# Optimization experiments

Hardware: AMD Instinct MI355X
Metric: run time of the kernel (lower is better)

The kernel has to match this reference:

```python
import jax, jax.numpy as jnp
import numpy as np

B, N, DIM, H, DH = 4, 8192, 1024, 8, 64
INNER = H * DH  # 512


def setup_inputs() -> dict:
    key = jax.random.key(0)
    ks = jax.random.split(key, 6)
    init = lambda k, shape, fan: (jax.random.normal(k, shape, jnp.float32) / np.sqrt(fan).astype(np.float32))
    return {
        "x": jax.random.normal(ks[0], (B, N, DIM), jnp.float32),
        "mask": jnp.ones((B, N), dtype=bool),
        "w_qkv": init(ks[1], (DIM, 3 * INNER), DIM),        # to_qkv (no bias)
        "w_q_logit": init(ks[2], (DH,), DH),                 # to_q_attn_logits
        "w_k_logit": init(ks[3], (DH,), DH),                 # to_k_attn_logits
        "w_r": init(ks[4], (DH, DH), DH),                    # to_r weight
        "b_r": jnp.zeros((DH,), jnp.float32),                # to_r bias
        "w_out": init(ks[5], (INNER, DIM), INNER),           # to_out weight
        "b_out": jnp.zeros((DIM,), jnp.float32),             # to_out bias
    }


def reference(x, mask, w_qkv, w_q_logit, w_k_logit, w_r, b_r, w_out, b_out):
    scale = DH ** -0.5
    neg = -jnp.finfo(x.dtype).max
    qkv = x @ w_qkv                                   # [b, n, 3*inner]
    q, k, v = jnp.split(qkv, 3, axis=-1)
    to_bhnd = lambda t: t.reshape(B, N, H, DH).transpose(0, 2, 1, 3)  # b h n d
    q, k, v = to_bhnd(q), to_bhnd(k), to_bhnd(v)
    m = mask[:, None, :]                              # b 1 n

    # query attention -> global query vector
    q_logits = jnp.einsum('bhnd,d->bhn', q, w_q_logit) * scale
    q_attn = jax.nn.softmax(jnp.where(m, q_logits, neg), axis=-1)
    global_q = jnp.einsum('bhn,bhnd->bhd', q_attn, q)  # b h d

    # key attention conditioned on global query -> global key vector
    k_mod = k * global_q[:, :, None, :]
    k_logits = jnp.einsum('bhnd,d->bhn', k_mod, w_k_logit) * scale
    k_attn = jax.nn.softmax(jnp.where(m, k_logits, neg), axis=-1)
    global_k = jnp.einsum('bhn,bhnd->bhd', k_attn, k)  # (k_aggr = original k)

    # value modulation + residual with q
    u = v * global_k[:, :, None, :]                   # b h n d
    r = jnp.einsum('bhnd,de->bhne', u, w_r) + b_r + q
    r = r.transpose(0, 2, 1, 3).reshape(B, N, INNER)  # b n (h d)
    return r @ w_out + b_out
```

## Files before the change

kernel.cpp:

```cpp
#include <hip/hip_runtime.h>
#include <hip/hip_bf16.h>
#include <cstdint>
#include <cstddef>

#define B_ 4
#define N_ 8192
#define DIM_ 1024
#define H_ 8
#define DH_ 64
#define INNER_ 512
#define QKVW 1536
#define NT_ 32768
#define CH_ 32
#define CROWS 256

typedef __bf16 bf16;
typedef __attribute__((ext_vector_type(8))) __bf16 bf16x8;
typedef __attribute__((ext_vector_type(4))) float f32x4;

__device__ __forceinline__ void gload_lds16(const void* g, void* l) {
  __builtin_amdgcn_global_load_lds((__attribute__((address_space(1))) void*)(g),
                                   (__attribute__((address_space(3))) void*)(l),
                                   16, 0, 0);
}

__global__ void k_convert(const float* __restrict__ src, bf16* __restrict__ dst, int n8) {
  int i = blockIdx.x * blockDim.x + threadIdx.x;
  int stride = gridDim.x * blockDim.x;
  for (; i < n8; i += stride) {
    const float4* p = reinterpret_cast<const float4*>(src) + (size_t)i * 2;
    float4 a = p[0], b = p[1];
    bf16x8 o;
    o[0] = (bf16)a.x; o[1] = (bf16)a.y; o[2] = (bf16)a.z; o[3] = (bf16)a.w;
    o[4] = (bf16)b.x; o[5] = (bf16)b.y; o[6] = (bf16)b.z; o[7] = (bf16)b.w;
    reinterpret_cast<bf16x8*>(dst)[i] = o;
  }
}

__global__ __launch_bounds__(256) void k_transpose_wqkv(const float* __restrict__ w,
                                                        bf16* __restrict__ wt) {
  __shared__ float t[32][33];
  const int n0 = (blockIdx.x % 48) * 32;
  const int k0 = (blockIdx.x / 48) * 32;
  const int c = threadIdx.x & 31, r8 = threadIdx.x >> 5;
#pragma unroll
  for (int i = 0; i < 4; ++i) {
    int rr = r8 + i * 8;
    t[rr][c] = w[(size_t)(k0 + rr) * QKVW + n0 + c];
  }
  __syncthreads();
#pragma unroll
  for (int i = 0; i < 4; ++i) {
    int rr = r8 + i * 8;
    wt[(size_t)(n0 + rr) * DIM_ + k0 + c] = (bf16)t[c][rr];
  }
}

#define BM 128
#define BN 128
#define BK 32

__global__ __launch_bounds__(256, 2) void k_gemm1(const bf16* __restrict__ A,
                                                  const bf16* __restrict__ BT,
                                                  bf16* __restrict__ C) {
  __shared__ bf16 As[BM * BK];
  __shared__ bf16 Bs[BN * BK];
  const int tid = threadIdx.x;
  const int lane = tid & 63;
  const int w = tid >> 6;
  const int wm = w >> 1, wn = w & 1;
  const int flat = blockIdx.y * gridDim.x + blockIdx.x;
  const int idx = (flat & 7) * ((gridDim.x * gridDim.y) >> 3) + (flat >> 3);
  const int m0 = (idx / gridDim.x) * BM;
  const int n0 = (idx % gridDim.x) * BN;
  const int r15 = lane & 15, g = lane >> 4;

  f32x4 acc[4][4] = {};

  for (int kt = 0; kt < DIM_ / BK; ++kt) {
    const int k0 = kt * BK;
#pragma unroll
    for (int i = 0; i < 2; ++i) {
      int f = i * 256 + tid;
      int row = f >> 2, ch = f & 3;
      gload_lds16(A + (size_t)(m0 + row) * DIM_ + k0 + ch * 8,
                  As + (size_t)(i * 256 + w * 64) * 8);
      gload_lds16(BT + (size_t)(n0 + row) * DIM_ + k0 + ch * 8,
                  Bs + (size_t)(i * 256 + w * 64) * 8);
    }
    __syncthreads();
    bf16x8 af[4], bfr[4];
#pragma unroll
    for (int mi = 0; mi < 4; ++mi)
      af[mi] = *reinterpret_cast<const bf16x8*>(As + (wm * 64 + mi * 16 + r15) * BK + g * 8);
#pragma unroll
    for (int ni = 0; ni < 4; ++ni)
      bfr[ni] = *reinterpret_cast<const bf16x8*>(Bs + (wn * 64 + ni * 16 + r15) * BK + g * 8);
#pragma unroll
    for (int mi = 0; mi < 4; ++mi)
#pragma unroll
      for (int ni = 0; ni < 4; ++ni)
        acc[mi][ni] = __builtin_amdgcn_mfma_f32_16x16x32_bf16(af[mi], bfr[ni], acc[mi][ni], 0, 0, 0);
    __syncthreads();
  }

#pragma unroll
  for (int mi = 0; mi < 4; ++mi)
#pragma unroll
    for (int ni = 0; ni < 4; ++ni) {
      int col = n0 + wn * 64 + ni * 16 + r15;
#pragma unroll
      for (int j = 0; j < 4; ++j) {
        int row = m0 + wm * 64 + mi * 16 + g * 4 + j;
        C[(size_t)row * QKVW + col] = (bf16)acc[mi][ni][j];
      }
    }
}

__global__ __launch_bounds__(256) void k_stats_part(const bf16* __restrict__ qkv,
                                                    const float* __restrict__ wql,
                                                    const float* __restrict__ wkl,
                                                    const float* __restrict__ partQ,
                                                    float* __restrict__ part,
                                                    int off, int mode) {
  __shared__ float lgs[CROWS];
  __shared__ float pl[CROWS];
  __shared__ float cfl[DH_];
  __shared__ float redm[4], reds[4];
  __shared__ float vacc[4][DH_];
  const int blk = blockIdx.x;
  const int bh = blk >> 5, ck = blk & 31;
  const int b = bh >> 3, h = bh & 7;
  const bf16* base = qkv + (size_t)(b * N_ + ck * CROWS) * QKVW + h * DH_ + off;
  const int tid = threadIdx.x, lane = tid & 63, w = tid >> 6;

  if (tid < DH_) {
    if (mode == 0) {
      cfl[tid] = wql[tid] * 0.125f;
    } else {
      const float* pp = partQ + (size_t)bh * CH_ * 66;
      float M = -3.4e38f;
#pragma unroll
      for (int c = 0; c < CH_; ++c) M = fmaxf(M, pp[c * 66 + 64]);
      float S = 0.f, v = 0.f;
#pragma unroll
      for (int c = 0; c < CH_; ++c) {
        float e = __expf(pp[c * 66 + 64] - M);
        S += pp[c * 66 + 65] * e;
        v += pp[c * 66 + tid] * e;
      }
      cfl[tid] = wkl[tid] * 0.125f * (v / S);
    }
  }
  __syncthreads();

  const int lr = tid & 7;
  const int rbase = tid >> 3;
  {
    const float c0 = cfl[lr * 8 + 0], c1 = cfl[lr * 8 + 1], c2 = cfl[lr * 8 + 2],
                c3 = cfl[lr * 8 + 3], c4 = cfl[lr * 8 + 4], c5 = cfl[lr * 8 + 5],
                c6 = cfl[lr * 8 + 6], c7 = cfl[lr * 8 + 7];
#pragma unroll
    for (int p = 0; p < 8; ++p) {
      int r = p * 32 + rbase;
      bf16x8 v = *reinterpret_cast<const bf16x8*>(base + (size_t)r * QKVW + lr * 8);
      float s = (float)v[0] * c0 + (float)v[1] * c1 + (float)v[2] * c2 + (float)v[3] * c3 +
                (float)v[4] * c4 + (float)v[5] * c5 + (float)v[6] * c6 + (float)v[7] * c7;
      s += __shfl_xor(s, 1);
      s += __shfl_xor(s, 2);
      s += __shfl_xor(s, 4);
      if (lr == 0) lgs[r] = s;
    }
  }
  __syncthreads();
  const float lg = lgs[tid];
  float m = lg;
#pragma unroll
  for (int d = 1; d < 64; d <<= 1) m = fmaxf(m, __shfl_xor(m, d));
  if (lane == 0) redm[w] = m;
  __syncthreads();
  const float M = fmaxf(fmaxf(redm[0], redm[1]), fmaxf(redm[2], redm[3]));
  float p = __expf(lg - M);
  pl[tid] = p;
  float s = p;
#pragma unroll
  for (int d = 1; d < 64; d <<= 1) s += __shfl_xor(s, d);
  if (lane == 0) reds[w] = s;
  __syncthreads();
  const float S = reds[0] + reds[1] + reds[2] + reds[3];
  float acc = 0.f;
#pragma unroll 8
  for (int r = w; r < CROWS; r += 4)
    acc += pl[r] * (float)base[(size_t)r * QKVW + lane];
  vacc[w][lane] = acc;
  __syncthreads();
  if (tid < DH_) {
    float v = vacc[0][tid] + vacc[1][tid] + vacc[2][tid] + vacc[3][tid];
    float* dst = part + ((size_t)bh * CH_ + ck) * 66;
    dst[tid] = v;
    if (tid == 0) { dst[64] = M; dst[65] = S; }
  }
}

__global__ void k_combine(const float* __restrict__ part, float* __restrict__ outv) {
  const int bh = blockIdx.x, d = threadIdx.x;
  const float* pp = part + (size_t)bh * CH_ * 66;
  float M = -3.4e38f;
#pragma unroll
  for (int c = 0; c < CH_; ++c) M = fmaxf(M, pp[c * 66 + 64]);
  float S = 0.f, v = 0.f;
#pragma unroll
  for (int c = 0; c < CH_; ++c) {
    float e = __expf(pp[c * 66 + 64] - M);
    S += pp[c * 66 + 65] * e;
    v += pp[c * 66 + d] * e;
  }
  outv[bh * DH_ + d] = v / S;
}

__global__ void k_P(const float* __restrict__ wr, const float* __restrict__ wout,
                    float* __restrict__ P) {
  int he = blockIdx.x;
  int h = he >> 6, e = he & 63;
  __shared__ float wrow[DH_];
  if (threadIdx.x < DH_) wrow[threadIdx.x] = wr[e * DH_ + threadIdx.x];
  __syncthreads();
  for (int o = threadIdx.x; o < DIM_; o += 256) {
    float s = 0.f;
#pragma unroll
    for (int d = 0; d < DH_; ++d) s += wrow[d] * wout[(size_t)(h * DH_ + d) * DIM_ + o];
    P[(size_t)he * DIM_ + o] = s;
  }
}

__global__ void k_bo2(const float* __restrict__ br, const float* __restrict__ wout,
                      const float* __restrict__ bout, float* __restrict__ bo2) {
  const int w = threadIdx.x >> 6, lane = threadIdx.x & 63;
  const int o = blockIdx.x * 4 + w;
  float s = 0.f;
#pragma unroll
  for (int j = lane; j < INNER_; j += 64) s += br[lane] * wout[(size_t)j * DIM_ + o];
#pragma unroll
  for (int d = 1; d < 64; d <<= 1) s += __shfl_xor(s, d);
  if (lane == 0) bo2[o] = s + bout[o];
}

__global__ void k_bt(const float* __restrict__ P, const float* __restrict__ gk,
                     const float* __restrict__ wout, bf16* __restrict__ BT) {
  int bo = blockIdx.x;
  int b = bo >> 10, o = bo & 1023;
  bf16* dst = BT + (size_t)bo * DIM_;
  for (int k = threadIdx.x; k < DIM_; k += 256) {
    float v;
    if (k < INNER_) {
      int h = k >> 6, e = k & 63;
      v = gk[(b * H_ + h) * DH_ + e] * P[(size_t)k * DIM_ + o];
    } else {
      v = wout[(size_t)(k - INNER_) * DIM_ + o];
    }
    dst[k] = (bf16)v;
  }
}

__global__ __launch_bounds__(256, 2) void k_gemm2(const bf16* __restrict__ qkv,
                                                  const bf16* __restrict__ BT,
                                                  const float* __restrict__ bo2,
                                                  float* __restrict__ out) {
  __shared__ bf16 As[BM * BK];
  __shared__ bf16 Bs[BN * BK];
  const int tid = threadIdx.x;
  const int lane = tid & 63;
  const int w = tid >> 6;
  const int wm = w >> 1, wn = w & 1;
  const int b = blockIdx.z;
  const int flat = blockIdx.y * gridDim.x + blockIdx.x;
  const int idx = (flat & 7) * ((gridDim.x * gridDim.y) >> 3) + (flat >> 3);
  const int m0 = (idx >> 3) * BM;
  const int n0 = (idx & 7) * BN;
  const int r15 = lane & 15, g = lane >> 4;
  const bf16* BTb = BT + (size_t)b * DIM_ * DIM_;

  f32x4 acc[4][4] = {};

  for (int kt = 0; kt < DIM_ / BK; ++kt) {
    const int k0 = kt * BK;
    const int koff = (k0 < INNER_) ? (2 * INNER_ + k0) : (k0 - INNER_);
#pragma unroll
    for (int i = 0; i < 2; ++i) {
      int f = i * 256 + tid;
      int row = f >> 2, ch = f & 3;
      gload_lds16(qkv + (size_t)(b * N_ + m0 + row) * QKVW + koff + ch * 8,
                  As + (size_t)(i * 256 + w * 64) * 8);
      gload_lds16(BTb + (size_t)(n0 + row) * DIM_ + k0 + ch * 8,
                  Bs + (size_t)(i * 256 + w * 64) * 8);
    }
    __syncthreads();
    bf16x8 af[4], bfr[4];
#pragma unroll
    for (int mi = 0; mi < 4; ++mi)
      af[mi] = *reinterpret_cast<const bf16x8*>(As + (wm * 64 + mi * 16 + r15) * BK + g * 8);
#pragma unroll
    for (int ni = 0; ni < 4; ++ni)
      bfr[ni] = *reinterpret_cast<const bf16x8*>(Bs + (wn * 64 + ni * 16 + r15) * BK + g * 8);
#pragma unroll
    for (int mi = 0; mi < 4; ++mi)
#pragma unroll
      for (int ni = 0; ni < 4; ++ni)
        acc[mi][ni] = __builtin_amdgcn_mfma_f32_16x16x32_bf16(af[mi], bfr[ni], acc[mi][ni], 0, 0, 0);
    __syncthreads();
  }

#pragma unroll
  for (int mi = 0; mi < 4; ++mi)
#pragma unroll
    for (int ni = 0; ni < 4; ++ni) {
      int col = n0 + wn * 64 + ni * 16 + r15;
      float bb = bo2[col];
#pragma unroll
      for (int j = 0; j < 4; ++j) {
        int row = m0 + wm * 64 + mi * 16 + g * 4 + j;
        out[(size_t)(b * N_ + row) * DIM_ + col] = acc[mi][ni][j] + bb;
      }
    }
}

extern "C" void kernel_launch(void* const* d_in, const int* in_sizes, int n_in,
                              void* d_out, int out_size, void* d_ws, size_t ws_size,
                              hipStream_t stream) {
  const float* x     = (const float*)d_in[0];
  const float* w_qkv = (const float*)d_in[2];
  const float* wql   = (const float*)d_in[3];
  const float* wkl   = (const float*)d_in[4];
  const float* w_r   = (const float*)d_in[5];
  const float* b_r   = (const float*)d_in[6];
  const float* w_out = (const float*)d_in[7];
  const float* b_out = (const float*)d_in[8];
  float* out = (float*)d_out;

  char* ws = (char*)d_ws;
  bf16* xb    = (bf16*)(ws);
  bf16* qkv   = (bf16*)(ws + 67108864);
  bf16* wqkvT = (bf16*)(ws + 167772160);
  bf16* BT    = (bf16*)(ws + 170917888);
  float* P    = (float*)(ws + 179306496);
  float* gk   = (float*)(ws + 181403648);
  float* bo2  = (float*)(ws + 181411840);
  float* partQ = (float*)BT;
  float* partK = (float*)(ws + 170917888 + 524288);

  k_convert<<<2048, 256, 0, stream>>>(x, xb, NT_ * DIM_ / 8);
  k_transpose_wqkv<<<48 * 32, 256, 0, stream>>>(w_qkv, wqkvT);
  dim3 g1(QKVW / BN, NT_ / BM);
  k_gemm1<<<g1, 256, 0, stream>>>(xb, wqkvT, qkv);

  k_stats_part<<<B_ * H_ * CH_, 256, 0, stream>>>(qkv, wql, wkl, partQ, partQ, 0, 0);
  k_stats_part<<<B_ * H_ * CH_, 256, 0, stream>>>(qkv, wql, wkl, partQ, partK, INNER_, 1);
  k_combine<<<B_ * H_, DH_, 0, stream>>>(partK, gk);

  k_P<<<512, 256, 0, stream>>>(w_r, w_out, P);
  k_bo2<<<256, 256, 0, stream>>>(b_r, w_out, b_out, bo2);
  k_bt<<<B_ * 1024, 256, 0, stream>>>(P, gk, w_out, BT);
  dim3 g2(DIM_ / BN, N_ / BM, B_);
  k_gemm2<<<g2, 256, 0, stream>>>(qkv, BT, bo2, out);
}
```

Before: 585.7 us.

## Fuse fp32-to-bf16 conversion of x into QKV GEMM A-tile loads

Removes the standalone conversion kernel that wrote a bf16 copy of x. The QKV GEMM now reads fp32 x directly, converts it to bf16 in registers and stores it to LDS, while B still uses async global-to-LDS loads. The GEMM is split into two launches over half the rows each, presumably to keep A tiles in cache. This saves a full write and reread of the activation, but the GEMM now reads twice as many bytes for A and uses synchronous loads plus conversion work in its inner loop.

```diff
diff --git a/kernel.cpp b/kernel.cpp
--- a/kernel.cpp
+++ b/kernel.cpp
@@ -24,19 +24,6 @@
                                    16, 0, 0);
 }
 
-__global__ void k_convert(const float* __restrict__ src, bf16* __restrict__ dst, int n8) {
-  int i = blockIdx.x * blockDim.x + threadIdx.x;
-  int stride = gridDim.x * blockDim.x;
-  for (; i < n8; i += stride) {
-    const float4* p = reinterpret_cast<const float4*>(src) + (size_t)i * 2;
-    float4 a = p[0], b = p[1];
-    bf16x8 o;
-    o[0] = (bf16)a.x; o[1] = (bf16)a.y; o[2] = (bf16)a.z; o[3] = (bf16)a.w;
-    o[4] = (bf16)b.x; o[5] = (bf16)b.y; o[6] = (bf16)b.z; o[7] = (bf16)b.w;
-    reinterpret_cast<bf16x8*>(dst)[i] = o;
-  }
-}
-
 __global__ __launch_bounds__(256) void k_transpose_wqkv(const float* __restrict__ w,
                                                         bf16* __restrict__ wt) {
   __shared__ float t[32][33];
@@ -60,9 +47,9 @@
 #define BN 128
 #define BK 32
 
-__global__ __launch_bounds__(256, 2) void k_gemm1(const bf16* __restrict__ A,
+__global__ __launch_bounds__(256, 2) void k_gemm1(const float* __restrict__ A32,
                                                   const bf16* __restrict__ BT,
-                                                  bf16* __restrict__ C) {
+                                                  bf16* __restrict__ C, int mbase) {
   __shared__ bf16 As[BM * BK];
   __shared__ bf16 Bs[BN * BK];
   const int tid = threadIdx.x;
@@ -71,9 +58,10 @@
   const int wm = w >> 1, wn = w & 1;
   const int flat = blockIdx.y * gridDim.x + blockIdx.x;
   const int idx = (flat & 7) * ((gridDim.x * gridDim.y) >> 3) + (flat >> 3);
-  const int m0 = (idx / gridDim.x) * BM;
+  const int m0 = mbase + (idx / gridDim.x) * BM;
   const int n0 = (idx % gridDim.x) * BN;
   const int r15 = lane & 15, g = lane >> 4;
+  const int arow = tid >> 1, aseg = tid & 1;
 
   f32x4 acc[4][4] = {};
 
@@ -83,10 +71,20 @@
     for (int i = 0; i < 2; ++i) {
       int f = i * 256 + tid;
       int row = f >> 2, ch = f & 3;
-      gload_lds16(A + (size_t)(m0 + row) * DIM_ + k0 + ch * 8,
-                  As + (size_t)(i * 256 + w * 64) * 8);
       gload_lds16(BT + (size_t)(n0 + row) * DIM_ + k0 + ch * 8,
                   Bs + (size_t)(i * 256 + w * 64) * 8);
+    }
+    {
+      const float4* ap = reinterpret_cast<const float4*>(
+          A32 + (size_t)(m0 + arow) * DIM_ + k0 + aseg * 16);
+      float4 f0 = ap[0], f1 = ap[1], f2 = ap[2], f3 = ap[3];
+      bf16x8 o0, o1;
+      o0[0] = (bf16)f0.x; o0[1] = (bf16)f0.y; o0[2] = (bf16)f0.z; o0[3] = (bf16)f0.w;
+      o0[4] = (bf16)f1.x; o0[5] = (bf16)f1.y; o0[6] = (bf16)f1.z; o0[7] = (bf16)f1.w;
+      o1[0] = (bf16)f2.x; o1[1] = (bf16)f2.y; o1[2] = (bf16)f2.z; o1[3] = (bf16)f2.w;
+      o1[4] = (bf16)f3.x; o1[5] = (bf16)f3.y; o1[6] = (bf16)f3.z; o1[7] = (bf16)f3.w;
+      *reinterpret_cast<bf16x8*>(As + arow * BK + aseg * 16) = o0;
+      *reinterpret_cast<bf16x8*>(As + arow * BK + aseg * 16 + 8) = o1;
     }
     __syncthreads();
     bf16x8 af[4], bfr[4];
@@ -338,20 +336,19 @@
   float* out = (float*)d_out;
 
   char* ws = (char*)d_ws;
-  bf16* xb    = (bf16*)(ws);
-  bf16* qkv   = (bf16*)(ws + 67108864);
-  bf16* wqkvT = (bf16*)(ws + 167772160);
-  bf16* BT    = (bf16*)(ws + 170917888);
-  float* P    = (float*)(ws + 179306496);
-  float* gk   = (float*)(ws + 181403648);
-  float* bo2  = (float*)(ws + 181411840);
+  bf16* qkv   = (bf16*)(ws);
+  bf16* wqkvT = (bf16*)(ws + 100663296);
+  bf16* BT    = (bf16*)(ws + 103809024);
+  float* P    = (float*)(ws + 112197632);
+  float* gk   = (float*)(ws + 114294784);
+  float* bo2  = (float*)(ws + 114302976);
   float* partQ = (float*)BT;
-  float* partK = (float*)(ws + 170917888 + 524288);
-
-  k_convert<<<2048, 256, 0, stream>>>(x, xb, NT_ * DIM_ / 8);
+  float* partK = (float*)(ws + 103809024 + 524288);
+
   k_transpose_wqkv<<<48 * 32, 256, 0, stream>>>(w_qkv, wqkvT);
-  dim3 g1(QKVW / BN, NT_ / BM);
-  k_gemm1<<<g1, 256, 0, stream>>>(xb, wqkvT, qkv);
+  dim3 g1(QKVW / BN, NT_ / BM / 2);
+  k_gemm1<<<g1, 256, 0, stream>>>(x, wqkvT, qkv, 0);
+  k_gemm1<<<g1, 256, 0, stream>>>(x, wqkvT, qkv, NT_ / 2);
 
   k_stats_part<<<B_ * H_ * CH_, 256, 0, stream>>>(qkv, wql, wkl, partQ, partQ, 0, 0);
   k_stats_part<<<B_ * H_ * CH_, 256, 0, stream>>>(qkv, wql, wkl, partQ, partK, INNER_, 1);
```

Measured after the change: 650.3 us. 11.0% more time.
